# Kernel optimization log

Hardware: AMD Instinct MI355X
Metric: run time of the kernel (lower is better)

## Reference

```python
import jax, jax.numpy as jnp
import numpy as np
import math

N = 100000      # nodes
E = 1600000     # edges (before self-loops)
F_IN = 512      # input features
H = 64          # hidden
C = 40          # classes
L = 4           # GCNII layers
ALPHA = 0.1
LAMDA = 0.5


def setup_inputs() -> dict:
    key = jax.random.key(0)
    ks = jax.random.split(key, 8)
    x = jax.random.normal(ks[0], (N, F_IN), jnp.float32)
    edge_index = jax.random.randint(ks[1], (2, E), 0, N)
    edge_weight = jax.random.uniform(ks[2], (E,), jnp.float32)
    W_in = jax.random.normal(ks[3], (F_IN, H), jnp.float32) * 0.05
    b_in = jnp.zeros((H,), jnp.float32)
    W_layers = jax.random.normal(ks[4], (L, H, H), jnp.float32) * 0.1
    W_out = jax.random.normal(ks[5], (H, C), jnp.float32) * 0.1
    b_out = jnp.zeros((C,), jnp.float32)
    return dict(x=x, edge_index=edge_index, edge_weight=edge_weight,
                W_in=W_in, b_in=b_in, W_layers=W_layers, W_out=W_out, b_out=b_out)


def _gcn_norm(edge_index, edge_weight, n):
    """Add self-loops (weight 1) and compute symmetric normalization D^-1/2 A D^-1/2."""
    loop = jnp.arange(n)
    src = jnp.concatenate([edge_index[0], loop])
    dst = jnp.concatenate([edge_index[1], loop])
    w = jnp.concatenate([edge_weight, jnp.ones((n,), edge_weight.dtype)])
    deg = jax.ops.segment_sum(w, dst, num_segments=n)
    dinv = jnp.where(deg > 0, jax.lax.rsqrt(deg), jnp.zeros_like(deg))
    norm = dinv[src] * w * dinv[dst]  # [E+N]
    return src, dst, norm


def reference(x, edge_index, edge_weight, W_in, b_in, W_layers, W_out, b_out):
    n = x.shape[0]
    src, dst, norm = _gcn_norm(edge_index, edge_weight, n)
    # input projection (dropout is identity in eval mode)
    h = jax.nn.relu(x @ W_in + b_in)  # [N, H]
    h0 = h
    for i in range(W_layers.shape[0]):
        beta = math.log(LAMDA / (i + 1) + 1.0)
        # sparse propagate: Ahat @ h via gather + segment_sum
        agg = jax.ops.segment_sum(norm[:, None] * h[src], dst, num_segments=n)  # [N, H]
        support = (1.0 - ALPHA) * agg + ALPHA * h0  # initial residual
        # identity mapping: beta * support @ W + (1 - beta) * support
        h = jax.nn.relu(beta * (support @ W_layers[i]) + (1.0 - beta) * support)
    out = h @ W_out + b_out  # [N, C]
    return jax.nn.log_softmax(out, axis=1)
```

## Files before the change

### kernel.cpp

```cpp
#include <hip/hip_runtime.h>
#include <math.h>

#define HD 64
#define FIN 512
#define NC 40

struct __align__(8) EdgeT { int s; float v; };

typedef __attribute__((ext_vector_type(8))) short bf16x8;
typedef __attribute__((ext_vector_type(8))) unsigned short u16x8;
typedef __attribute__((ext_vector_type(4))) float f32x4;

__device__ __forceinline__ float bf2f(ushort u) {
    return __uint_as_float(((unsigned int)u) << 16);
}
__device__ __forceinline__ ushort f2bf(float f) {
    unsigned int u = __float_as_uint(f);
    unsigned int r = (u + 0x7fffu + ((u >> 16) & 1u)) >> 16;
    return (ushort)r;
}


__global__ __launch_bounds__(256) void prep_kernel(uint* packed8, int n,
        const float* __restrict__ Win, ushort* __restrict__ Wf,
        const float* __restrict__ Wlay, ushort* __restrict__ Wf2, int L,
        const float* __restrict__ Wo, const float* __restrict__ bo,
        ushort* __restrict__ Wfo, float* __restrict__ bo_pad) {
    int i = blockIdx.x * 256 + threadIdx.x;
    if (i < 8 * n) packed8[i] = (i < n) ? (1u << 21) : 0u;
    if (i < FIN * HD) {
        int j = i & 7, l = (i >> 3) & 63, t = (i >> 9) & 3, c = i >> 11;
        int k = c * 32 + ((l >> 4) * 8) + j;
        Wf[i] = f2bf(Win[k * HD + t * 16 + (l & 15)]);
    }
    if (i < L * HD * HD) {
        int li = i >> 12, ii = i & 4095;
        int j = ii & 7, l = (ii >> 3) & 63, t = (ii >> 9) & 3, c = (ii >> 11) & 1;
        int k = c * 32 + ((l >> 4) * 8) + j;
        Wf2[i] = f2bf(Wlay[(size_t)li * HD * HD + k * HD + t * 16 + (l & 15)]);
    }
    if (i < HD * HD) {
        int j = i & 7, l = (i >> 3) & 63, t = (i >> 9) & 3, c = (i >> 11) & 1;
        int k = c * 32 + ((l >> 4) * 8) + j;
        int col = t * 16 + (l & 15);
        Wfo[i] = (col < NC) ? f2bf(Wo[k * NC + col]) : (ushort)0;
    }
    if (i < HD) bo_pad[i] = (i < NC) ? bo[i] : 0.f;
}


__global__ __launch_bounds__(256) void histproj_kernel(
        const int* __restrict__ dst, const float* __restrict__ w,
        uint* packed8, ushort* __restrict__ rank, int E, int n,
        const float* __restrict__ x, const ushort* __restrict__ Wf,
        const float* __restrict__ bias, ushort* __restrict__ h0,
        int npb, int k) {
    const int q = blockIdx.x / k;
    const int r = blockIdx.x - q * k;
    if (r != 0) {
        int hid = q * (k - 1) + (r - 1);
        int i1 = hid * 512 + threadIdx.x;
        int i2 = i1 + 256;
        if (i1 < E) {
            int d = dst[i1];
            int c = i1 & 7;
            uint add = (1u << 26) | (uint)(w[i1] * 2097152.0f);
            uint old = atomicAdd(&packed8[(size_t)c * n + d], add);
            rank[i1] = (ushort)(old >> 26);
        }
        if (i2 < E) {
            int d = dst[i2];
            int c = i2 & 7;
            uint add = (1u << 26) | (uint)(w[i2] * 2097152.0f);
            uint old = atomicAdd(&packed8[(size_t)c * n + d], add);
            rank[i2] = (ushort)(old >> 26);
        }
        return;
    }
    const int lane = threadIdx.x & 63;
    const int wave = threadIdx.x >> 6;
    const int row = lane & 15;
    const int g = lane >> 4;
    const int base = q * 64 + wave * 16;

    f32x4 acc[4];
#pragma unroll
    for (int t = 0; t < 4; ++t) acc[t] = (f32x4){0.f, 0.f, 0.f, 0.f};

    int nodeA = base + row;
    if (nodeA >= n) nodeA = n - 1;
    const float* xr = x + (size_t)nodeA * FIN + g * 8;

    for (int c = 0; c < 16; ++c) {
        bf16x8 afr;
        float4 v0 = *(const float4*)(xr + c * 32);
        float4 v1 = *(const float4*)(xr + c * 32 + 4);
        afr[0] = (short)f2bf(v0.x); afr[1] = (short)f2bf(v0.y);
        afr[2] = (short)f2bf(v0.z); afr[3] = (short)f2bf(v0.w);
        afr[4] = (short)f2bf(v1.x); afr[5] = (short)f2bf(v1.y);
        afr[6] = (short)f2bf(v1.z); afr[7] = (short)f2bf(v1.w);
#pragma unroll
        for (int t = 0; t < 4; ++t) {
            bf16x8 bfr = *(const bf16x8*)(Wf + ((size_t)(c * 4 + t) * 64 + lane) * 8);
            acc[t] = __builtin_amdgcn_mfma_f32_16x16x32_bf16(afr, bfr, acc[t], 0, 0, 0);
        }
    }

    float bj[4];
#pragma unroll
    for (int t = 0; t < 4; ++t) bj[t] = bias[t * 16 + row];
#pragma unroll
    for (int rr = 0; rr < 4; ++rr) {
        int node = base + g * 4 + rr;
        if (node < n) {
#pragma unroll
            for (int t = 0; t < 4; ++t) {
                float v = fmaxf(acc[t][rr] + bj[t], 0.f);
                h0[(size_t)node * HD + t * 16 + row] = f2bf(v);
            }
        }
    }
}

__global__ __launch_bounds__(256) void post_kernel(const uint* __restrict__ packed8,
        float* __restrict__ dinv, uint2* __restrict__ cbase,
        int* __restrict__ row_ptr, int* __restrict__ bsums, int n) {
    __shared__ int s[256];
    int t = threadIdx.x;
    int i = blockIdx.x * 256 + t;
    int cnt = 0;
    if (i < n) {
        int c[8];
        unsigned long long fx = 0;
#pragma unroll
        for (int k = 0; k < 8; ++k) {
            uint p = packed8[(size_t)k * n + i];
            c[k] = (int)(p >> 26);
            fx += (p & 0x3FFFFFFu);
        }
        float deg = (float)((double)fx * (1.0 / 2097152.0));
        dinv[i] = rsqrtf(deg);
        int b = 0; uint lo = 0, hi = 0;
#pragma unroll
        for (int k = 0; k < 4; ++k) { lo |= ((uint)b) << (8 * k); b += c[k]; }
#pragma unroll
        for (int k = 0; k < 4; ++k) { hi |= ((uint)b) << (8 * k); b += c[4 + k]; }
        cbase[i] = make_uint2(lo, hi);
        cnt = b;
    }
    s[t] = cnt; __syncthreads();
    for (int off = 1; off < 256; off <<= 1) {
        int u = (t >= off) ? s[t - off] : 0;
        __syncthreads();
        s[t] += u;
        __syncthreads();
    }
    if (i < n) row_ptr[i] = s[t] - cnt;
    if (t == 255) bsums[blockIdx.x] = s[255];
}

__global__ __launch_bounds__(512) void scan_top_kernel(int* bsums, int nb) {
    __shared__ int s[512];
    int t = threadIdx.x;
    int v = (t < nb) ? bsums[t] : 0;
    s[t] = v; __syncthreads();
    for (int off = 1; off < 512; off <<= 1) {
        int u = (t >= off) ? s[t - off] : 0;
        __syncthreads();
        s[t] += u;
        __syncthreads();
    }
    if (t < nb) bsums[t] = s[t] - v;
}

__global__ __launch_bounds__(256) void scan_add_kernel(int* __restrict__ row_ptr,
        const int* __restrict__ bsums, int n, int E) {
    int i = blockIdx.x * 256 + threadIdx.x;
    if (i < n) row_ptr[i] += bsums[blockIdx.x];
    if (i == 0) row_ptr[n] = E;
}

__global__ __launch_bounds__(256) void scatter_kernel(const int* __restrict__ src,
        const int* __restrict__ dst, const float* __restrict__ w,
        const float* __restrict__ dinv, const int* __restrict__ row_ptr,
        const uint2* __restrict__ cbase, const ushort* __restrict__ rank,
        EdgeT* __restrict__ ed, int E) {
    int i = blockIdx.x * 256 + threadIdx.x;
    if (i < E) {
        int s = src[i], d = dst[i];
        int c = i & 7;
        uint2 cb = cbase[d];
        int base = (int)(((c < 4) ? (cb.x >> (8 * c)) : (cb.y >> (8 * (c - 4)))) & 0xffu);
        int pos = row_ptr[d] + base + (int)rank[i];
        EdgeT e; e.s = s; e.v = dinv[s] * w[i] * dinv[d];
        ed[pos] = e;
    }
}


__global__ __launch_bounds__(256) void layerm_kernel(const ushort* __restrict__ h_in,
        const ushort* __restrict__ h0, ushort* __restrict__ h_out,
        const ushort* __restrict__ Wf2, const float* __restrict__ dinv,
        const int* __restrict__ row_ptr, const EdgeT* __restrict__ ed,
        float beta, int n) {
    __shared__ ushort S[4][32 * 72];
    const int lane = threadIdx.x & 63;
    const int wave = threadIdx.x >> 6;
    ushort* Sw = S[wave];
    const int wbase = (blockIdx.x * 4 + wave) * 32;
    const int gs = lane >> 3;
    const int fl = (lane & 7) * 8;

#pragma unroll
    for (int p = 0; p < 4; ++p) {
        int node = wbase + p * 8 + gs;
        int nc = (node < n) ? node : n - 1;
        float di = dinv[nc];
        float sw = di * di;
        u16x8 us = *(const u16x8*)(h_in + (size_t)nc * HD + fl);
        float a[8], b[8];
#pragma unroll
        for (int j = 0; j < 8; ++j) { a[j] = sw * bf2f((ushort)us[j]); b[j] = 0.f; }

        int e = row_ptr[nc], end = row_ptr[nc + 1];
        for (; e + 4 <= end; e += 4) {
            EdgeT E0 = ed[e], E1 = ed[e + 1], E2 = ed[e + 2], E3 = ed[e + 3];
            u16x8 u0 = *(const u16x8*)(h_in + (size_t)E0.s * HD + fl);
            u16x8 u1 = *(const u16x8*)(h_in + (size_t)E1.s * HD + fl);
            u16x8 u2 = *(const u16x8*)(h_in + (size_t)E2.s * HD + fl);
            u16x8 u3 = *(const u16x8*)(h_in + (size_t)E3.s * HD + fl);
#pragma unroll
            for (int j = 0; j < 8; ++j) {
                a[j] = fmaf(E0.v, bf2f((ushort)u0[j]), a[j]);
                b[j] = fmaf(E1.v, bf2f((ushort)u1[j]), b[j]);
                a[j] = fmaf(E2.v, bf2f((ushort)u2[j]), a[j]);
                b[j] = fmaf(E3.v, bf2f((ushort)u3[j]), b[j]);
            }
        }
        for (; e < end; ++e) {
            EdgeT E0 = ed[e];
            u16x8 u0 = *(const u16x8*)(h_in + (size_t)E0.s * HD + fl);
#pragma unroll
            for (int j = 0; j < 8; ++j) a[j] = fmaf(E0.v, bf2f((ushort)u0[j]), a[j]);
        }

        u16x8 uh = *(const u16x8*)(h0 + (size_t)nc * HD + fl);
        u16x8 r;
#pragma unroll
        for (int j = 0; j < 8; ++j)
            r[j] = f2bf(fmaf(0.9f, a[j] + b[j], 0.1f * bf2f((ushort)uh[j])));
        *(u16x8*)(Sw + (p * 8 + gs) * 72 + fl) = r;
    }

    asm volatile("s_waitcnt lgkmcnt(0)" ::: "memory");
    __builtin_amdgcn_wave_barrier();
    __builtin_amdgcn_sched_barrier(0);

    const int row = lane & 15;
    const int g = lane >> 4;
    f32x4 acc[2][4];
#pragma unroll
    for (int m = 0; m < 2; ++m)
#pragma unroll
        for (int t = 0; t < 4; ++t) acc[m][t] = (f32x4){0.f, 0.f, 0.f, 0.f};

#pragma unroll
    for (int c = 0; c < 2; ++c) {
        bf16x8 afr[2];
#pragma unroll
        for (int m = 0; m < 2; ++m)
            afr[m] = *(const bf16x8*)(Sw + (m * 16 + row) * 72 + c * 32 + g * 8);
#pragma unroll
        for (int t = 0; t < 4; ++t) {
            bf16x8 bfr = *(const bf16x8*)(Wf2 + ((size_t)(c * 4 + t) * 64 + lane) * 8);
            acc[0][t] = __builtin_amdgcn_mfma_f32_16x16x32_bf16(afr[0], bfr, acc[0][t], 0, 0, 0);
            acc[1][t] = __builtin_amdgcn_mfma_f32_16x16x32_bf16(afr[1], bfr, acc[1][t], 0, 0, 0);
        }
    }

    const float ombeta = 1.f - beta;
#pragma unroll
    for (int m = 0; m < 2; ++m)
#pragma unroll
        for (int r = 0; r < 4; ++r) {
            int node = wbase + m * 16 + g * 4 + r;
            if (node < n) {
#pragma unroll
                for (int t = 0; t < 4; ++t) {
                    float sup = bf2f(Sw[(m * 16 + g * 4 + r) * 72 + t * 16 + row]);
                    float v = fmaxf(fmaf(beta, acc[m][t][r], ombeta * sup), 0.f);
                    h_out[(size_t)node * HD + t * 16 + row] = f2bf(v);
                }
            }
        }
}


__global__ __launch_bounds__(256) void outm_kernel(const ushort* __restrict__ A,
        const ushort* __restrict__ Wfo, const float* __restrict__ bo_pad,
        float* __restrict__ outp, int n) {
    const int lane = threadIdx.x & 63;
    const int wave = threadIdx.x >> 6;
    const int row = lane & 15;
    const int g = lane >> 4;
    const int base = blockIdx.x * 128 + wave * 32;

    f32x4 acc[2][4];
#pragma unroll
    for (int m = 0; m < 2; ++m)
#pragma unroll
        for (int t = 0; t < 4; ++t) acc[m][t] = (f32x4){0.f, 0.f, 0.f, 0.f};

#pragma unroll
    for (int c = 0; c < 2; ++c) {
        bf16x8 afr[2];
#pragma unroll
        for (int m = 0; m < 2; ++m) {
            int node = base + m * 16 + row;
            if (node >= n) node = n - 1;
            afr[m] = *(const bf16x8*)(A + (size_t)node * HD + c * 32 + g * 8);
        }
#pragma unroll
        for (int t = 0; t < 4; ++t) {
            bf16x8 bfr = *(const bf16x8*)(Wfo + ((size_t)(c * 4 + t) * 64 + lane) * 8);
            acc[0][t] = __builtin_amdgcn_mfma_f32_16x16x32_bf16(afr[0], bfr, acc[0][t], 0, 0, 0);
            acc[1][t] = __builtin_amdgcn_mfma_f32_16x16x32_bf16(afr[1], bfr, acc[1][t], 0, 0, 0);
        }
    }

    float bj[4];
#pragma unroll
    for (int t = 0; t < 4; ++t) bj[t] = bo_pad[t * 16 + row];
    const bool v2 = (row < 8);
#pragma unroll
    for (int m = 0; m < 2; ++m)
#pragma unroll
        for (int r = 0; r < 4; ++r) {
            float lo[3];
            lo[0] = acc[m][0][r] + bj[0];
            lo[1] = acc[m][1][r] + bj[1];
            lo[2] = acc[m][2][r] + bj[2];
            float mx = fmaxf(lo[0], lo[1]);
            if (v2) mx = fmaxf(mx, lo[2]);
#pragma unroll
            for (int off = 1; off < 16; off <<= 1)
                mx = fmaxf(mx, __shfl_xor(mx, off, 64));
            float s = __expf(lo[0] - mx) + __expf(lo[1] - mx);
            if (v2) s += __expf(lo[2] - mx);
#pragma unroll
            for (int off = 1; off < 16; off <<= 1)
                s += __shfl_xor(s, off, 64);
            float lse = __logf(s);
            int node = base + m * 16 + g * 4 + r;
            if (node < n) {
                outp[(size_t)node * NC + row] = lo[0] - mx - lse;
                outp[(size_t)node * NC + 16 + row] = lo[1] - mx - lse;
                if (v2) outp[(size_t)node * NC + 32 + row] = lo[2] - mx - lse;
            }
        }
}


extern "C" void kernel_launch(void* const* d_in, const int* in_sizes, int n_in,
                              void* d_out, int out_size, void* d_ws, size_t ws_size,
                              hipStream_t stream) {
    const float* x        = (const float*)d_in[0];
    const int*   eidx     = (const int*)d_in[1];
    const float* ew       = (const float*)d_in[2];
    const float* W_in     = (const float*)d_in[3];
    const float* b_in     = (const float*)d_in[4];
    const float* W_layers = (const float*)d_in[5];
    const float* W_out    = (const float*)d_in[6];
    const float* b_out    = (const float*)d_in[7];
    float* out = (float*)d_out;

    const int N = in_sizes[0] / FIN;
    const int E = in_sizes[2];
    const int L = in_sizes[5] / (HD * HD);
    const int* src = eidx;
    const int* dst = eidx + E;

    size_t off = 0;
    auto carve = [&](size_t bytes) {
        void* p = (char*)d_ws + off;
        off += (bytes + 255) & ~(size_t)255;
        return p;
    };
    uint*   packed8 = (uint*) carve((size_t)N * 8 * 4);
    float*  dinv    = (float*)carve((size_t)N * 4);
    uint2*  cbase   = (uint2*)carve((size_t)N * 8);
    int*    row_ptr = (int*)  carve((size_t)(N + 1) * 4);
    int*    bsums   = (int*)  carve(512 * 4);
    float*  bo_pad  = (float*)carve((size_t)HD * 4);
    ushort* Wf      = (ushort*)carve((size_t)FIN * HD * 2);
    ushort* Wf2     = (ushort*)carve((size_t)L * HD * HD * 2);
    ushort* Wfo     = (ushort*)carve((size_t)HD * HD * 2);
    ushort* rank    = (ushort*)carve((size_t)E * 2);
    EdgeT*  ed      = (EdgeT*)carve((size_t)E * 8);
    ushort* h0      = (ushort*)carve((size_t)N * HD * 2);
    ushort* hA      = (ushort*)carve((size_t)N * HD * 2);
    ushort* hB      = (ushort*)carve((size_t)N * HD * 2);
    (void)ws_size;

    const int NB = (N + 255) / 256;
    const int EB = (E + 255) / 256;
    const int NPB = (N + 63) / 64;
    const int HB  = (E + 511) / 512;
    const int K   = (NPB + HB + NPB - 1) / NPB;
    const int GRID = NPB * K;

    prep_kernel<<<(8 * N + 255) / 256, 256, 0, stream>>>(packed8, N, W_in, Wf,
                                                         W_layers, Wf2, L,
                                                         W_out, b_out, Wfo, bo_pad);
    histproj_kernel<<<GRID, 256, 0, stream>>>(dst, ew, packed8, rank, E, N,
                                              x, Wf, b_in, h0, NPB, K);
    post_kernel<<<NB, 256, 0, stream>>>(packed8, dinv, cbase, row_ptr, bsums, N);
    scan_top_kernel<<<1, 512, 0, stream>>>(bsums, NB);
    scan_add_kernel<<<NB, 256, 0, stream>>>(row_ptr, bsums, N, E);
    scatter_kernel<<<EB, 256, 0, stream>>>(src, dst, ew, dinv, row_ptr, cbase, rank, ed, E);

    const int LB = (N + 127) / 128;
    const ushort* cur = h0;
    ushort* bufs[2] = { hA, hB };
    for (int i = 0; i < L; ++i) {
        float beta = logf(0.5f / (float)(i + 1) + 1.0f);
        ushort* nxt = bufs[i & 1];
        layerm_kernel<<<LB, 256, 0, stream>>>(cur, h0, nxt, Wf2 + (size_t)i * HD * HD,
                                              dinv, row_ptr, ed, beta, N);
        cur = nxt;
    }

    outm_kernel<<<LB, 256, 0, stream>>>(cur, Wfo, bo_pad, out, N);
}
```

Before: 333.2 us.

## Fold identity mapping into layer weights, merge scan kernels, widen gather unroll

The layer weights are pre-scaled as beta*W + (1-beta)*I, so each layer epilogue only applies a ReLU to the MFMA result and no longer rereads support from shared memory. The two top-level scan kernels become one, where each block reduces the preceding block sums itself, removing a single-block launch. The edge gather loop is unrolled to 8 in-flight neighbour loads for more memory parallelism, and histogram blocks each handle 1024 edges instead of 512. The risks are extra register pressure from the deeper unroll and support now entering the matmul in bf16 precision.

```diff
diff --git a/kernel.cpp b/kernel.cpp
--- a/kernel.cpp
+++ b/kernel.cpp
@@ -37,7 +37,11 @@
         int li = i >> 12, ii = i & 4095;
         int j = ii & 7, l = (ii >> 3) & 63, t = (ii >> 9) & 3, c = (ii >> 11) & 1;
         int k = c * 32 + ((l >> 4) * 8) + j;
-        Wf2[i] = f2bf(Wlay[(size_t)li * HD * HD + k * HD + t * 16 + (l & 15)]);
+        int col = t * 16 + (l & 15);
+        float beta = logf(0.5f / (float)(li + 1) + 1.0f);
+        float v = beta * Wlay[(size_t)li * HD * HD + k * HD + col] +
+                  ((k == col) ? (1.f - beta) : 0.f);
+        Wf2[i] = f2bf(v);
     }
     if (i < HD * HD) {
         int j = i & 7, l = (i >> 3) & 63, t = (i >> 9) & 3, c = (i >> 11) & 1;
@@ -59,21 +63,17 @@
     const int r = blockIdx.x - q * k;
     if (r != 0) {
         int hid = q * (k - 1) + (r - 1);
-        int i1 = hid * 512 + threadIdx.x;
-        int i2 = i1 + 256;
-        if (i1 < E) {
-            int d = dst[i1];
-            int c = i1 & 7;
-            uint add = (1u << 26) | (uint)(w[i1] * 2097152.0f);
-            uint old = atomicAdd(&packed8[(size_t)c * n + d], add);
-            rank[i1] = (ushort)(old >> 26);
-        }
-        if (i2 < E) {
-            int d = dst[i2];
-            int c = i2 & 7;
-            uint add = (1u << 26) | (uint)(w[i2] * 2097152.0f);
-            uint old = atomicAdd(&packed8[(size_t)c * n + d], add);
-            rank[i2] = (ushort)(old >> 26);
+        int i0 = hid * 1024 + threadIdx.x;
+#pragma unroll
+        for (int p = 0; p < 4; ++p) {
+            int i = i0 + p * 256;
+            if (i < E) {
+                int d = dst[i];
+                int c = i & 7;
+                uint add = (1u << 26) | (uint)(w[i] * 2097152.0f);
+                uint old = atomicAdd(&packed8[(size_t)c * n + d], add);
+                rank[i] = (ushort)(old >> 26);
+            }
         }
         return;
     }
@@ -159,24 +159,22 @@
     if (t == 255) bsums[blockIdx.x] = s[255];
 }
 
-__global__ __launch_bounds__(512) void scan_top_kernel(int* bsums, int nb) {
-    __shared__ int s[512];
-    int t = threadIdx.x;
-    int v = (t < nb) ? bsums[t] : 0;
+__global__ __launch_bounds__(256) void scanadd_kernel(int* __restrict__ row_ptr,
+        const int* __restrict__ bsums, int n, int E) {
+    __shared__ int s[256];
+    const int b = blockIdx.x;
+    const int t = threadIdx.x;
+    int v = (t < b) ? bsums[t] : 0;
+    if (t + 256 < b) v += bsums[t + 256];
     s[t] = v; __syncthreads();
-    for (int off = 1; off < 512; off <<= 1) {
-        int u = (t >= off) ? s[t - off] : 0;
+#pragma unroll
+    for (int off = 128; off >= 1; off >>= 1) {
+        if (t < off) s[t] += s[t + off];
         __syncthreads();
-        s[t] += u;
-        __syncthreads();
-    }
-    if (t < nb) bsums[t] = s[t] - v;
-}
-
-__global__ __launch_bounds__(256) void scan_add_kernel(int* __restrict__ row_ptr,
-        const int* __restrict__ bsums, int n, int E) {
-    int i = blockIdx.x * 256 + threadIdx.x;
-    if (i < n) row_ptr[i] += bsums[blockIdx.x];
+    }
+    int prefix = s[0];
+    int i = b * 256 + t;
+    if (i < n) row_ptr[i] += prefix;
     if (i == 0) row_ptr[n] = E;
 }
 
@@ -201,8 +199,7 @@
 __global__ __launch_bounds__(256) void layerm_kernel(const ushort* __restrict__ h_in,
         const ushort* __restrict__ h0, ushort* __restrict__ h_out,
         const ushort* __restrict__ Wf2, const float* __restrict__ dinv,
-        const int* __restrict__ row_ptr, const EdgeT* __restrict__ ed,
-        float beta, int n) {
+        const int* __restrict__ row_ptr, const EdgeT* __restrict__ ed, int n) {
     __shared__ ushort S[4][32 * 72];
     const int lane = threadIdx.x & 63;
     const int wave = threadIdx.x >> 6;
@@ -223,21 +220,34 @@
         for (int j = 0; j < 8; ++j) { a[j] = sw * bf2f((ushort)us[j]); b[j] = 0.f; }
 
         int e = row_ptr[nc], end = row_ptr[nc + 1];
-        for (; e + 4 <= end; e += 4) {
-            EdgeT E0 = ed[e], E1 = ed[e + 1], E2 = ed[e + 2], E3 = ed[e + 3];
+        for (; e + 8 <= end; e += 8) {
+            EdgeT Ex[8];
+            u16x8 ux[8];
+#pragma unroll
+            for (int k = 0; k < 8; ++k) Ex[k] = ed[e + k];
+#pragma unroll
+            for (int k = 0; k < 8; ++k)
+                ux[k] = *(const u16x8*)(h_in + (size_t)Ex[k].s * HD + fl);
+#pragma unroll
+            for (int k = 0; k < 8; k += 2) {
+#pragma unroll
+                for (int j = 0; j < 8; ++j) {
+                    a[j] = fmaf(Ex[k].v,     bf2f((ushort)ux[k][j]),     a[j]);
+                    b[j] = fmaf(Ex[k + 1].v, bf2f((ushort)ux[k + 1][j]), b[j]);
+                }
+            }
+        }
+        for (; e + 2 <= end; e += 2) {
+            EdgeT E0 = ed[e], E1 = ed[e + 1];
             u16x8 u0 = *(const u16x8*)(h_in + (size_t)E0.s * HD + fl);
             u16x8 u1 = *(const u16x8*)(h_in + (size_t)E1.s * HD + fl);
-            u16x8 u2 = *(const u16x8*)(h_in + (size_t)E2.s * HD + fl);
-            u16x8 u3 = *(const u16x8*)(h_in + (size_t)E3.s * HD + fl);
 #pragma unroll
             for (int j = 0; j < 8; ++j) {
                 a[j] = fmaf(E0.v, bf2f((ushort)u0[j]), a[j]);
                 b[j] = fmaf(E1.v, bf2f((ushort)u1[j]), b[j]);
-                a[j] = fmaf(E2.v, bf2f((ushort)u2[j]), a[j]);
-                b[j] = fmaf(E3.v, bf2f((ushort)u3[j]), b[j]);
-            }
-        }
-        for (; e < end; ++e) {
+            }
+        }
+        if (e < end) {
             EdgeT E0 = ed[e];
             u16x8 u0 = *(const u16x8*)(h_in + (size_t)E0.s * HD + fl);
 #pragma unroll
@@ -278,7 +288,6 @@
         }
     }
 
-    const float ombeta = 1.f - beta;
 #pragma unroll
     for (int m = 0; m < 2; ++m)
 #pragma unroll
@@ -287,8 +296,7 @@
             if (node < n) {
 #pragma unroll
                 for (int t = 0; t < 4; ++t) {
-                    float sup = bf2f(Sw[(m * 16 + g * 4 + r) * 72 + t * 16 + row]);
-                    float v = fmaxf(fmaf(beta, acc[m][t][r], ombeta * sup), 0.f);
+                    float v = fmaxf(acc[m][t][r], 0.f);
                     h_out[(size_t)node * HD + t * 16 + row] = f2bf(v);
                 }
             }
@@ -405,7 +413,7 @@
     const int NB = (N + 255) / 256;
     const int EB = (E + 255) / 256;
     const int NPB = (N + 63) / 64;
-    const int HB  = (E + 511) / 512;
+    const int HB  = (E + 1023) / 1024;
     const int K   = (NPB + HB + NPB - 1) / NPB;
     const int GRID = NPB * K;
 
@@ -415,18 +423,16 @@
     histproj_kernel<<<GRID, 256, 0, stream>>>(dst, ew, packed8, rank, E, N,
                                               x, Wf, b_in, h0, NPB, K);
     post_kernel<<<NB, 256, 0, stream>>>(packed8, dinv, cbase, row_ptr, bsums, N);
-    scan_top_kernel<<<1, 512, 0, stream>>>(bsums, NB);
-    scan_add_kernel<<<NB, 256, 0, stream>>>(row_ptr, bsums, N, E);
+    scanadd_kernel<<<NB, 256, 0, stream>>>(row_ptr, bsums, N, E);
     scatter_kernel<<<EB, 256, 0, stream>>>(src, dst, ew, dinv, row_ptr, cbase, rank, ed, E);
 
     const int LB = (N + 127) / 128;
     const ushort* cur = h0;
     ushort* bufs[2] = { hA, hB };
     for (int i = 0; i < L; ++i) {
-        float beta = logf(0.5f / (float)(i + 1) + 1.0f);
         ushort* nxt = bufs[i & 1];
         layerm_kernel<<<LB, 256, 0, stream>>>(cur, h0, nxt, Wf2 + (size_t)i * HD * HD,
-                                              dinv, row_ptr, ed, beta, N);
+                                              dinv, row_ptr, ed, N);
         cur = nxt;
     }
 
```

Measured after the change: 412.0 us. 1.24x slower.
